# Performance work log

Measured on AMD Instinct MI355X. Metric: run time of the kernel, lower is better.

Reference implementation:

```python
import jax, jax.numpy as jnp
import numpy as np

K = 16  # num_neighbors
L = 3   # stacked PointTransformer layers


def _mlp2(x, w1, b1, w2, b2):
    return jax.nn.relu(x @ w1 + b1) @ w2 + b2


def setup_inputs() -> dict:
    key = jax.random.key(0)
    ks = jax.random.split(key, 10)
    B, N, D = 2, 8192, 3
    HP, HA = 32, 12  # pos_mlp hidden, attn_mlp hidden (3*4)
    f = lambda k, shp, s: jax.random.normal(k, shp, dtype=jnp.float32) * s
    return {
        "feats": f(ks[0], (B, N, D), 1.0),
        "pos": f(ks[1], (B, N, 3), 1.0),
        "mask": jnp.ones((B, N), dtype=bool),  # unused by PT.forward
        "w_qkv": f(ks[2], (L, D, 3 * D), 1.0 / np.sqrt(D)),
        "pos_w1": f(ks[3], (L, 3, HP), 1.0 / np.sqrt(3.0)),
        "pos_b1": jnp.zeros((L, HP), jnp.float32),
        "pos_w2": f(ks[4], (L, HP, D), 1.0 / np.sqrt(HP)),
        "pos_b2": jnp.zeros((L, D), jnp.float32),
        "attn_w1": f(ks[5], (L, D, HA), 1.0 / np.sqrt(D)),
        "attn_b1": jnp.zeros((L, HA), jnp.float32),
        "attn_w2": f(ks[6], (L, HA, D), 1.0 / np.sqrt(HA)),
        "attn_b2": jnp.zeros((L, D), jnp.float32),
        "lin_w": f(ks[7], (D, 2), 1.0 / np.sqrt(D)),
        "lin_b": jnp.zeros((2,), jnp.float32),
    }


def reference(feats, pos, mask, w_qkv, pos_w1, pos_b1, pos_w2, pos_b2,
              attn_w1, attn_b1, attn_w2, attn_b2, lin_w, lin_b):
    # kNN indices from pairwise squared distances (monotonic in the norm the
    # original uses, so topk-smallest gives identical neighbor sets).
    sq = jnp.sum(pos * pos, axis=-1)                               # [B,N]
    d2 = sq[:, :, None] + sq[:, None, :] - 2.0 * jnp.einsum('bic,bjc->bij', pos, pos)
    _, idx = jax.lax.top_k(-d2, K)                                 # [B,N,K]

    gather = jax.vmap(lambda t, i: t[i])                           # [B,N,d],[B,N,K]->[B,N,K,d]
    pos_j = gather(pos, idx)                                       # [B,N,K,3]
    rel_pos = pos[:, :, None, :] - pos_j                           # [B,N,K,3]

    h = feats
    for l in range(L):
        qkv = h @ w_qkv[l]                                         # [B,N,9]
        q, k, v = jnp.split(qkv, 3, axis=-1)
        k_j = gather(k, idx)                                       # [B,N,K,3]
        v_j = gather(v, idx)
        rel_emb = _mlp2(rel_pos, pos_w1[l], pos_b1[l], pos_w2[l], pos_b2[l])
        qk_rel = q[:, :, None, :] - k_j
        sim = _mlp2(qk_rel + rel_emb, attn_w1[l], attn_b1[l], attn_w2[l], attn_b2[l])
        attn = jax.nn.softmax(sim, axis=-2)                        # softmax over neighbors
        agg = jnp.einsum('bijd,bijd->bid', attn, v_j + rel_emb)    # [B,N,3]
        h = jax.nn.sigmoid(agg)
    out = h @ lin_w + lin_b                                        # [B,N,2]
    return jax.nn.softmax(out, axis=2)
```

## Files before the change

kernel.cpp:

```cpp
#include <hip/hip_runtime.h>
#include <math.h>

#define N_PTS 8192
#define BATCH 2
#define KNB 16
#define NQ (BATCH * N_PTS)

#define H    0.35f
#define INVH (1.0f / 0.35f)
#define NC   30
#define LBOX (0.5f * H * NC)
#define NCELL (NC * NC * NC)
#define MCELL (2 * NCELL)
#define NROW1 9
#define NROWT 43
#define NCHK 8
#define CHKP (N_PTS / NCHK)
#define SCANG 8192
#define MERGG 1024
#define WCAP 8192
#define FINF 3.4e38f

typedef unsigned long long u64;

__device__ __forceinline__ float med3f(float a, float b, float c) {
#if __has_builtin(__builtin_amdgcn_fmed3f)
    return __builtin_amdgcn_fmed3f(a, b, c);
#else
    return fmaxf(fminf(a, b), fminf(fmaxf(a, b), c));
#endif
}

__device__ __forceinline__ unsigned sortable(float x) {
    unsigned u = __float_as_uint(x);
    return u ^ ((unsigned)((int)u >> 31) | 0x80000000u);
}

__device__ __forceinline__ void ins_u64(u64 (&pk)[KNB], u64 key) {
    if (key < pk[0]) {
#pragma unroll
        for (int s = 0; s < KNB; ++s) {
            const u64 ds1 = (s < KNB - 1) ? pk[s + 1] : 0ull;
            const bool c0 = key < pk[s];
            const bool c1 = key < ds1;
            pk[s] = c1 ? ds1 : (c0 ? key : pk[s]);
        }
    }
}

__device__ __forceinline__ void sort16_desc_u64(u64 (&a)[KNB]) {
#pragma unroll
    for (int k = 2; k <= 16; k <<= 1) {
#pragma unroll
        for (int j = k >> 1; j > 0; j >>= 1) {
#pragma unroll
            for (int i = 0; i < 16; ++i) {
                const int l = i ^ j;
                if (l > i) {
                    const bool dirDesc = ((i & k) == 0);
                    const u64 mx = a[i] > a[l] ? a[i] : a[l];
                    const u64 mn = a[i] > a[l] ? a[l] : a[i];
                    a[i] = dirDesc ? mx : mn;
                    a[l] = dirDesc ? mn : mx;
                }
            }
        }
    }
}

__device__ __forceinline__ void merge64_u64(u64 (&pk)[KNB]) {
#pragma unroll
    for (int mm = 1; mm <= 32; mm <<= 1) {
        u64 L[KNB];
#pragma unroll
        for (int i = 0; i < KNB; ++i) {
            const u64 a = pk[i];
            const u64 c = __shfl_xor(pk[KNB - 1 - i], mm);
            L[i] = a < c ? a : c;
        }
#pragma unroll
        for (int dd = 8; dd >= 1; dd >>= 1) {
#pragma unroll
            for (int i = 0; i < KNB; ++i) {
                if ((i & dd) == 0) {
                    const u64 hi = L[i] > L[i | dd] ? L[i] : L[i | dd];
                    const u64 lo = L[i] > L[i | dd] ? L[i | dd] : L[i];
                    L[i] = hi; L[i | dd] = lo;
                }
            }
        }
#pragma unroll
        for (int i = 0; i < KNB; ++i) pk[i] = L[i];
    }
}

__global__ __launch_bounds__(256) void kcount(const float* __restrict__ pos,
                                              int* __restrict__ cnt,
                                              int* __restrict__ cellid) {
    const int g = blockIdx.x * 256 + threadIdx.x;
    const int b = g >> 13;
    const float x = pos[g * 3 + 0], y = pos[g * 3 + 1], z = pos[g * 3 + 2];
    int cx = (int)floorf((x + LBOX) * INVH); cx = min(max(cx, 0), NC - 1);
    int cy = (int)floorf((y + LBOX) * INVH); cy = min(max(cy, 0), NC - 1);
    int cz = (int)floorf((z + LBOX) * INVH); cz = min(max(cz, 0), NC - 1);
    const int c = (((b * NC) + cz) * NC + cy) * NC + cx;
    cellid[g] = c;
    atomicAdd(&cnt[c], 1);
}

__global__ __launch_bounds__(1024) void kscan1(const int* __restrict__ cnt,
                                               int* __restrict__ scanned,
                                               int* __restrict__ bsum) {
    __shared__ int sh[1024];
    const int t = threadIdx.x;
    const int idx = blockIdx.x * 1024 + t;
    int v = (idx < MCELL) ? cnt[idx] : 0;
    sh[t] = v;
    __syncthreads();
    for (int off = 1; off < 1024; off <<= 1) {
        const int add = (t >= off) ? sh[t - off] : 0;
        __syncthreads();
        sh[t] += add;
        __syncthreads();
    }
    if (idx < MCELL) scanned[idx] = sh[t];
    if (t == 1023) bsum[blockIdx.x] = sh[1023];
}

__global__ __launch_bounds__(1024) void kscan2(const int* __restrict__ scanned,
                                               const int* __restrict__ bsum,
                                               int* __restrict__ cell_start) {
    __shared__ int soff;
    const int t = threadIdx.x;
    const int blk = blockIdx.x;
    const int idx = blk * 1024 + t;
    if (t == 0) {
        int s = 0;
        for (int k = 0; k < blk; ++k) s += bsum[k];
        soff = s;
    }
    __syncthreads();
    if (idx < MCELL) cell_start[idx + 1] = scanned[idx] + soff;
    if (idx == 0) cell_start[0] = 0;
}

__global__ __launch_bounds__(256) void kscatter(const float* __restrict__ pos,
                                                const int* __restrict__ cellid,
                                                const int* __restrict__ cell_start,
                                                int* __restrict__ cnt2,
                                                float4* __restrict__ spp,
                                                int* __restrict__ sidx) {
    const int g = blockIdx.x * 256 + threadIdx.x;
    const int c = cellid[g];
    const int off = atomicAdd(&cnt2[c], 1);
    const int p = cell_start[c] + off;
    const float x = pos[g * 3 + 0], y = pos[g * 3 + 1], z = pos[g * 3 + 2];
    spp[p] = make_float4(-2.f * x, -2.f * y, -2.f * z, fmaf(x, x, fmaf(y, y, z * z)));
    sidx[p] = g & (N_PTS - 1);
}

__global__ __launch_bounds__(64, 4) void ksearch_fast(const float4* __restrict__ spp,
                                                      const int* __restrict__ sidx,
                                                      const int* __restrict__ cs,
                                                      int* __restrict__ knn,
                                                      int* __restrict__ ovf_list,
                                                      int* __restrict__ ovf_cnt) {
    __shared__ int rstL[4][NROWT];
    __shared__ int psL[4][NROWT + 1];
    const int tid = threadIdx.x;
    const int li  = tid & 15;
    const int gq  = tid >> 4;
    const int sq  = blockIdx.x * 4 + gq;
    const int b   = sq >> 13;

    {
        __shared__ int cntL[4][NROWT];
        for (int t = tid; t < 4 * NROWT; t += 64) {
            const int q = t / NROWT, r = t % NROWT;
            const int sq2 = blockIdx.x * 4 + q;
            const int b2  = sq2 >> 13;
            const float4 m2 = spp[sq2];
            const float px = -0.5f * m2.x, py = -0.5f * m2.y, pz = -0.5f * m2.z;
            int c2x = (int)floorf((px + LBOX) * INVH); c2x = min(max(c2x, 0), NC - 1);
            int c2y = (int)floorf((py + LBOX) * INVH); c2y = min(max(c2y, 0), NC - 1);
            int c2z = (int)floorf((pz + LBOX) * INVH); c2z = min(max(c2z, 0), NC - 1);

            int st = 0, en = 0;
            int z, y, xlo, xhi;
            bool ok = true;
            if (r < NROW1) {
                z = c2z + r / 3 - 1;
                y = c2y + (r % 3) - 1;
                xlo = max(c2x - 1, 0); xhi = min(c2x + 1, NC - 1);
            } else {
                const int rr = r - NROW1;
                if (rr < 10) {
                    z = c2z + (rr < 5 ? -2 : 2);
                    y = c2y + (rr % 5) - 2;
                    xlo = max(c2x - 2, 0); xhi = min(c2x + 2, NC - 1);
                } else if (rr < 16) {
                    const int k = rr - 10;
                    z = c2z + (k % 3) - 1;
                    y = c2y + (k < 3 ? -2 : 2);
                    xlo = max(c2x - 2, 0); xhi = min(c2x + 2, NC - 1);
                } else {
                    const int k = rr - 16;
                    const int m = k % 9;
                    z = c2z + m / 3 - 1;
                    y = c2y + (m % 3) - 1;
                    const int xx = c2x + (k < 9 ? -2 : 2);
                    xlo = xhi = xx;
                    ok = (xx >= 0) && (xx < NC);
                }
            }
            if (ok && z >= 0 && z < NC && y >= 0 && y < NC) {
                const int rowb = (((b2 * NC) + z) * NC + y) * NC;
                st = cs[rowb + xlo];
                en = cs[rowb + xhi + 1];
            }
            rstL[q][r] = st; cntL[q][r] = en - st;
        }
        __syncthreads();
        if (tid < 4) {
            int acc = 0;
            psL[tid][0] = 0;
            for (int r = 0; r < NROWT; ++r) { acc += cntL[tid][r]; psL[tid][r + 1] = acc; }
        }
        __syncthreads();
    }

    const float4 me = spp[sq];
    const float qx = -0.5f * me.x, qy = -0.5f * me.y, qz = -0.5f * me.z;
    const float qsq = me.w;
    int cx = (int)floorf((qx + LBOX) * INVH); cx = min(max(cx, 0), NC - 1);
    int cy = (int)floorf((qy + LBOX) * INVH); cy = min(max(cy, 0), NC - 1);
    int cz = (int)floorf((qz + LBOX) * INVH); cz = min(max(cz, 0), NC - 1);

    const int tot1 = psL[gq][NROW1];
    const int tot2 = psL[gq][NROWT];

    float d[KNB];
#pragma unroll
    for (int k = 0; k < KNB; ++k) d[k] = FINF;

    int row = 0;
    int t = li;

    auto scan1_flat = [&](int limit) {
        while (t < limit) {
            int pp[8]; bool vv[8];
#pragma unroll
            for (int u = 0; u < 8; ++u) {
                const int tt = t + u * 16;
                vv[u] = (tt < limit);
                int p = sq;
                if (vv[u]) {
                    while (tt >= psL[gq][row + 1]) ++row;
                    p = rstL[gq][row] + (tt - psL[gq][row]);
                }
                pp[u] = p;
            }
            float4 v[8];
#pragma unroll
            for (int u = 0; u < 8; ++u) v[u] = spp[pp[u]];
#pragma unroll
            for (int u = 0; u < 8; ++u) {
                const float x = vv[u] ? fmaf(qx, v[u].x, fmaf(qy, v[u].y, fmaf(qz, v[u].z, v[u].w)))
                                      : FINF;
                if (x < d[0]) {
#pragma unroll
                    for (int s = 0; s < KNB - 1; ++s) d[s] = med3f(d[s], d[s + 1], x);
                    d[KNB - 1] = fminf(d[KNB - 1], x);
                }
            }
            t += 128;
        }
    };

    auto boundtest = [&](int R) -> bool {
        const float bxl = fmaf((float)(cx - R), H, -LBOX);
        const float bxh = fmaf((float)(cx + R + 1), H, -LBOX);
        const float byl = fmaf((float)(cy - R), H, -LBOX);
        const float byh = fmaf((float)(cy + R + 1), H, -LBOX);
        const float bzl = fmaf((float)(cz - R), H, -LBOX);
        const float bzh = fmaf((float)(cz + R + 1), H, -LBOX);
        const float m = fminf(fminf(fminf(qx - bxl, bxh - qx),
                                    fminf(qy - byl, byh - qy)),
                              fminf(qz - bzl, bzh - qz));
        if (!(m > 0.f)) return false;
        const float Bf = fmaf(m, m, -1e-4f) - qsq;
        int c = 0;
#pragma unroll
        for (int k = 0; k < KNB; ++k) c += (d[k] <= Bf) ? 1 : 0;
#pragma unroll
        for (int off = 1; off < 16; off <<= 1) c += __shfl_xor(c, off);
        return c >= KNB;
    };

    scan1_flat(tot1);
    const bool done1 = boundtest(1);
    bool ovf = false;
    if (!done1) {
        scan1_flat(tot2);
        if (!boundtest(2)) ovf = true;
    }
    if (ovf) {
        if (li == 0) { const int s2 = atomicAdd(ovf_cnt, 1); ovf_list[s2] = sq; }
        return;
    }
    const int tot = done1 ? tot1 : tot2;

#pragma unroll
    for (int mm = 1; mm <= 8; mm <<= 1) {
        float L[KNB];
#pragma unroll
        for (int i = 0; i < KNB; ++i)
            L[i] = fminf(d[i], __shfl_xor(d[KNB - 1 - i], mm));
#pragma unroll
        for (int dd = 8; dd >= 1; dd >>= 1) {
#pragma unroll
            for (int i = 0; i < KNB; ++i) {
                if ((i & dd) == 0) {
                    const float hi = fmaxf(L[i], L[i | dd]);
                    const float lo = fminf(L[i], L[i | dd]);
                    L[i] = hi; L[i | dd] = lo;
                }
            }
        }
#pragma unroll
        for (int i = 0; i < KNB; ++i) d[i] = L[i];
    }
    const float thr = d[0];

    u64 pk[KNB];
#pragma unroll
    for (int k = 0; k < KNB; ++k) pk[k] = 0xFFFFFFFFFFFFFFFFull;

    row = 0;
    int t2 = li;
    while (t2 < tot) {
        int pp[8]; bool vv[8];
#pragma unroll
        for (int u = 0; u < 8; ++u) {
            const int tt = t2 + u * 16;
            vv[u] = (tt < tot);
            int p = sq;
            if (vv[u]) {
                while (tt >= psL[gq][row + 1]) ++row;
                p = rstL[gq][row] + (tt - psL[gq][row]);
            }
            pp[u] = p;
        }
        float4 v[8];
#pragma unroll
        for (int u = 0; u < 8; ++u) v[u] = spp[pp[u]];
#pragma unroll
        for (int u = 0; u < 8; ++u) {
            const float x = vv[u] ? fmaf(qx, v[u].x, fmaf(qy, v[u].y, fmaf(qz, v[u].z, v[u].w)))
                                  : FINF;
            if (x <= thr) {
                ins_u64(pk, ((u64)sortable(x) << 32) | (unsigned)sidx[pp[u]]);
            }
        }
        t2 += 128;
    }

#pragma unroll
    for (int mm = 1; mm <= 8; mm <<= 1) {
        u64 L[KNB];
#pragma unroll
        for (int i = 0; i < KNB; ++i) {
            const u64 a = pk[i];
            const u64 c = __shfl_xor(pk[KNB - 1 - i], mm);
            L[i] = a < c ? a : c;
        }
#pragma unroll
        for (int dd = 8; dd >= 1; dd >>= 1) {
#pragma unroll
            for (int i = 0; i < KNB; ++i) {
                if ((i & dd) == 0) {
                    const u64 hi = L[i] > L[i | dd] ? L[i] : L[i | dd];
                    const u64 lo = L[i] > L[i | dd] ? L[i | dd] : L[i];
                    L[i] = hi; L[i | dd] = lo;
                }
            }
        }
#pragma unroll
        for (int i = 0; i < KNB; ++i) pk[i] = L[i];
    }

    const int qorig = sidx[sq];
    const int obase = ((b << 13) + qorig) * KNB;
    u64 sel = pk[0];
#pragma unroll
    for (int s = 1; s < KNB; ++s) sel = (li == s) ? pk[s] : sel;
    knn[obase + li] = (int)(unsigned)(sel & 0xFFFFFFFFull);
}

__global__ __launch_bounds__(64, 4) void kslow_scan(const float4* __restrict__ spp,
                                                    const int* __restrict__ sidx,
                                                    const int* __restrict__ ovf_list,
                                                    const int* __restrict__ ovf_cnt,
                                                    u64* __restrict__ pbuf) {
    const int lane = threadIdx.x;
    const int ntask = min(*ovf_cnt, WCAP) * NCHK;

    for (int task = blockIdx.x; task < ntask; task += SCANG) {
        const int w = task >> 3;
        const int c = task & (NCHK - 1);
        const int sq = ovf_list[w];
        const int b  = sq >> 13;
        const float4 me = spp[sq];
        const float qx = -0.5f * me.x, qy = -0.5f * me.y, qz = -0.5f * me.z;
        const int cbase = (b << 13) + c * CHKP;

        u64 pk[KNB];
#pragma unroll
        for (int t0 = 0; t0 < 2; ++t0) {
            const int tb = cbase + lane + t0 * 512;
            float4 v[8];
            int id[8];
#pragma unroll
            for (int u = 0; u < 8; ++u) v[u] = spp[tb + u * 64];
#pragma unroll
            for (int u = 0; u < 8; ++u) id[u] = sidx[tb + u * 64];
#pragma unroll
            for (int u = 0; u < 8; ++u) {
                const float x = fmaf(qx, v[u].x, fmaf(qy, v[u].y, fmaf(qz, v[u].z, v[u].w)));
                pk[t0 * 8 + u] = ((u64)sortable(x) << 32) | (unsigned)id[u];
            }
        }

        sort16_desc_u64(pk);
        merge64_u64(pk);

        u64 sel = pk[0];
#pragma unroll
        for (int s = 1; s < KNB; ++s) sel = (lane == s) ? pk[s] : sel;
        if (lane < KNB) pbuf[(size_t)task * KNB + lane] = sel;
    }
}

__global__ __launch_bounds__(64) void kslow_merge(const float4* __restrict__ spp,
                                                  const int* __restrict__ sidx,
                                                  int* __restrict__ knn,
                                                  const int* __restrict__ ovf_list,
                                                  const int* __restrict__ ovf_cnt,
                                                  const u64* __restrict__ pbuf) {
    const int lane = threadIdx.x;
    const int nov = *ovf_cnt;

    for (int w = blockIdx.x; w < nov; w += MERGG) {
        const int sq = ovf_list[w];
        const int b  = sq >> 13;

        u64 pk[KNB];
#pragma unroll
        for (int k = 0; k < KNB; ++k) pk[k] = 0xFFFFFFFFFFFFFFFFull;

        if (w < WCAP) {
            const u64 a0 = pbuf[(size_t)w * (NCHK * KNB) + lane];
            const u64 a1 = pbuf[(size_t)w * (NCHK * KNB) + 64 + lane];
            ins_u64(pk, a0);
            ins_u64(pk, a1);
        } else {
            const float4 me = spp[sq];
            const float qx = -0.5f * me.x, qy = -0.5f * me.y, qz = -0.5f * me.z;
            const int base = b << 13;
            unsigned smax = 0xFFFFFFFFu;
            for (int t = lane; t < N_PTS; t += 64) {
                const float4 v = spp[base + t];
                const float x = fmaf(qx, v.x, fmaf(qy, v.y, fmaf(qz, v.z, v.w)));
                const unsigned sx = sortable(x);
                if (sx <= smax) {
                    ins_u64(pk, ((u64)sx << 32) | (unsigned)sidx[base + t]);
                    smax = (unsigned)(pk[0] >> 32);
                }
            }
        }

        merge64_u64(pk);

        const int qorig = sidx[sq];
        const int obase = ((b << 13) + qorig) * KNB;
        u64 sel = pk[0];
#pragma unroll
        for (int s = 1; s < KNB; ++s) sel = (lane == s) ? pk[s] : sel;
        if (lane < KNB) knn[obase + lane] = (int)(unsigned)(sel & 0xFFFFFFFFull);
    }
}

__global__ __launch_bounds__(256) void pt_layer_f(const float* __restrict__ hin,
                                                  const float* __restrict__ pos,
                                                  const int* __restrict__ knn,
                                                  const float* __restrict__ wqkv,
                                                  const float* __restrict__ pw1,
                                                  const float* __restrict__ pb1,
                                                  const float* __restrict__ pw2,
                                                  const float* __restrict__ pb2,
                                                  const float* __restrict__ aw1,
                                                  const float* __restrict__ ab1,
                                                  const float* __restrict__ aw2,
                                                  const float* __restrict__ ab2,
                                                  float* __restrict__ hout,
                                                  const float* __restrict__ lw,
                                                  const float* __restrict__ lb,
                                                  float* __restrict__ out,
                                                  int last) {
    const int gt = blockIdx.x * 256 + threadIdx.x;
    const int qg = gt >> 4;
    const int j  = gt & 15;
    const int b  = qg >> 13;
    const int jj = knn[qg * KNB + j] & (N_PTS - 1);
    const int g  = (b << 13) + jj;

    const float hi0 = hin[qg * 3 + 0], hi1 = hin[qg * 3 + 1], hi2 = hin[qg * 3 + 2];
    const float hj0 = hin[g * 3 + 0],  hj1 = hin[g * 3 + 1],  hj2 = hin[g * 3 + 2];
    const float rx = pos[qg * 3 + 0] - pos[g * 3 + 0];
    const float ry = pos[qg * 3 + 1] - pos[g * 3 + 1];
    const float rz = pos[qg * 3 + 2] - pos[g * 3 + 2];

    const float q0 = fmaf(hi0, wqkv[0], fmaf(hi1, wqkv[9],  hi2 * wqkv[18]));
    const float q1 = fmaf(hi0, wqkv[1], fmaf(hi1, wqkv[10], hi2 * wqkv[19]));
    const float q2 = fmaf(hi0, wqkv[2], fmaf(hi1, wqkv[11], hi2 * wqkv[20]));
    const float k0 = fmaf(hj0, wqkv[3], fmaf(hj1, wqkv[12], hj2 * wqkv[21]));
    const float k1 = fmaf(hj0, wqkv[4], fmaf(hj1, wqkv[13], hj2 * wqkv[22]));
    const float k2 = fmaf(hj0, wqkv[5], fmaf(hj1, wqkv[14], hj2 * wqkv[23]));
    const float v0 = fmaf(hj0, wqkv[6], fmaf(hj1, wqkv[15], hj2 * wqkv[24]));
    const float v1 = fmaf(hj0, wqkv[7], fmaf(hj1, wqkv[16], hj2 * wqkv[25]));
    const float v2 = fmaf(hj0, wqkv[8], fmaf(hj1, wqkv[17], hj2 * wqkv[26]));

    float e0 = pb2[0], e1 = pb2[1], e2 = pb2[2];
#pragma unroll
    for (int hh = 0; hh < 32; ++hh) {
        float t = fmaf(rx, pw1[hh], fmaf(ry, pw1[32 + hh], fmaf(rz, pw1[64 + hh], pb1[hh])));
        t = fmaxf(t, 0.0f);
        e0 = fmaf(t, pw2[hh * 3 + 0], e0);
        e1 = fmaf(t, pw2[hh * 3 + 1], e1);
        e2 = fmaf(t, pw2[hh * 3 + 2], e2);
    }

    const float x0 = q0 - k0 + e0;
    const float x1 = q1 - k1 + e1;
    const float x2 = q2 - k2 + e2;

    float s0 = ab2[0], s1 = ab2[1], s2 = ab2[2];
#pragma unroll
    for (int hh = 0; hh < 12; ++hh) {
        float t = fmaf(x0, aw1[hh], fmaf(x1, aw1[12 + hh], fmaf(x2, aw1[24 + hh], ab1[hh])));
        t = fmaxf(t, 0.0f);
        s0 = fmaf(t, aw2[hh * 3 + 0], s0);
        s1 = fmaf(t, aw2[hh * 3 + 1], s1);
        s2 = fmaf(t, aw2[hh * 3 + 2], s2);
    }

    const float w0 = v0 + e0, w1 = v1 + e1, w2 = v2 + e2;

    float m0 = s0, m1 = s1, m2 = s2;
#pragma unroll
    for (int off = 1; off < 16; off <<= 1) {
        m0 = fmaxf(m0, __shfl_xor(m0, off));
        m1 = fmaxf(m1, __shfl_xor(m1, off));
        m2 = fmaxf(m2, __shfl_xor(m2, off));
    }
    const float ex0 = __expf(s0 - m0), ex1 = __expf(s1 - m1), ex2 = __expf(s2 - m2);
    float n0 = ex0 * w0, n1 = ex1 * w1, n2 = ex2 * w2;
    float den0 = ex0, den1 = ex1, den2 = ex2;
#pragma unroll
    for (int off = 1; off < 16; off <<= 1) {
        den0 += __shfl_xor(den0, off); n0 += __shfl_xor(n0, off);
        den1 += __shfl_xor(den1, off); n1 += __shfl_xor(n1, off);
        den2 += __shfl_xor(den2, off); n2 += __shfl_xor(n2, off);
    }

    if (j == 0) {
        const float h0 = 1.f / (1.f + __expf(-(n0 / den0)));
        const float h1 = 1.f / (1.f + __expf(-(n1 / den1)));
        const float h2 = 1.f / (1.f + __expf(-(n2 / den2)));
        if (!last) {
            hout[qg * 3 + 0] = h0;
            hout[qg * 3 + 1] = h1;
            hout[qg * 3 + 2] = h2;
        } else {
            const float o0 = fmaf(h0, lw[0], fmaf(h1, lw[2], fmaf(h2, lw[4], lb[0])));
            const float o1 = fmaf(h0, lw[1], fmaf(h1, lw[3], fmaf(h2, lw[5], lb[1])));
            const float mm = fmaxf(o0, o1);
            const float ea = __expf(o0 - mm), eb = __expf(o1 - mm);
            const float inv = 1.f / (ea + eb);
            out[qg * 2 + 0] = ea * inv;
            out[qg * 2 + 1] = eb * inv;
        }
    }
}

extern "C" void kernel_launch(void* const* d_in, const int* in_sizes, int n_in,
                              void* d_out, int out_size, void* d_ws, size_t ws_size,
                              hipStream_t stream) {
    const float* feats = (const float*)d_in[0];
    const float* pos   = (const float*)d_in[1];
    const float* wqkv = (const float*)d_in[3];
    const float* pw1  = (const float*)d_in[4];
    const float* pb1  = (const float*)d_in[5];
    const float* pw2  = (const float*)d_in[6];
    const float* pb2  = (const float*)d_in[7];
    const float* aw1  = (const float*)d_in[8];
    const float* ab1  = (const float*)d_in[9];
    const float* aw2  = (const float*)d_in[10];
    const float* ab2  = (const float*)d_in[11];
    const float* lw   = (const float*)d_in[12];
    const float* lb   = (const float*)d_in[13];
    float* out = (float*)d_out;

    size_t o = 0;
    auto take = [&](size_t bytes) { size_t r = o; o += (bytes + 15) & ~(size_t)15; return r; };
    const size_t o_cnt   = take((size_t)(2 * MCELL + 4) * 4);
    const size_t o_scan  = take((size_t)MCELL * 4);
    const size_t o_cs    = take((size_t)(MCELL + 1) * 4);
    const size_t o_bsum  = take((size_t)256 * 4);
    const size_t o_cid   = take((size_t)NQ * 4);
    const size_t o_spp   = take((size_t)NQ * 16);
    const size_t o_sidx  = take((size_t)NQ * 4);
    const size_t o_knn   = take((size_t)NQ * KNB * 4);
    const size_t o_ovfl  = take((size_t)NQ * 4);
    const size_t o_hA    = take((size_t)NQ * 3 * 4);
    const size_t o_hB    = take((size_t)NQ * 3 * 4);
    const size_t o_pbuf  = take((size_t)WCAP * NCHK * KNB * 8);
    if (ws_size < o) return;

    char* ws = (char*)d_ws;
    int*    cnt     = (int*)(ws + o_cnt);
    int*    cnt2    = cnt + MCELL;
    int*    ovf_cnt = cnt + 2 * MCELL;
    int*    scan  = (int*)(ws + o_scan);
    int*    cs    = (int*)(ws + o_cs);
    int*    bsum  = (int*)(ws + o_bsum);
    int*    cid   = (int*)(ws + o_cid);
    float4* spp   = (float4*)(ws + o_spp);
    int*    sidx  = (int*)(ws + o_sidx);
    int*    knn   = (int*)(ws + o_knn);
    int*    ovfl  = (int*)(ws + o_ovfl);
    float*  hA    = (float*)(ws + o_hA);
    float*  hB    = (float*)(ws + o_hB);
    u64*    pbuf  = (u64*)(ws + o_pbuf);

    const int nscan = (MCELL + 1023) / 1024;

    hipMemsetAsync(cnt, 0, (size_t)(2 * MCELL + 1) * 4, stream);
    kcount<<<NQ / 256, 256, 0, stream>>>(pos, cnt, cid);
    kscan1<<<nscan, 1024, 0, stream>>>(cnt, scan, bsum);
    kscan2<<<nscan, 1024, 0, stream>>>(scan, bsum, cs);
    kscatter<<<NQ / 256, 256, 0, stream>>>(pos, cid, cs, cnt2, spp, sidx);
    ksearch_fast<<<NQ / 4, 64, 0, stream>>>(spp, sidx, cs, knn, ovfl, ovf_cnt);
    kslow_scan<<<SCANG, 64, 0, stream>>>(spp, sidx, ovfl, ovf_cnt, pbuf);
    kslow_merge<<<MERGG, 64, 0, stream>>>(spp, sidx, knn, ovfl, ovf_cnt, pbuf);

    pt_layer_f<<<NQ * 16 / 256, 256, 0, stream>>>(feats, pos, knn,
        wqkv + 0, pw1 + 0, pb1 + 0, pw2 + 0, pb2 + 0,
        aw1 + 0, ab1 + 0, aw2 + 0, ab2 + 0,
        hA, lw, lb, out, 0);
    pt_layer_f<<<NQ * 16 / 256, 256, 0, stream>>>(hA, pos, knn,
        wqkv + 27, pw1 + 96, pb1 + 32, pw2 + 96, pb2 + 3,
        aw1 + 36, ab1 + 12, aw2 + 36, ab2 + 3,
        hB, lw, lb, out, 0);
    pt_layer_f<<<NQ * 16 / 256, 256, 0, stream>>>(hB, pos, knn,
        wqkv + 54, pw1 + 192, pb1 + 64, pw2 + 192, pb2 + 6,
        aw1 + 72, ab1 + 24, aw2 + 72, ab2 + 6,
        hB, lw, lb, out, 1);
}
```

Before: 132.4 us.

## Fuse slow kNN fallback into one two-pass threshold kernel

Replaces the two-kernel chunked fallback search (per-chunk u64 bitonic sort into a partial buffer, then a merge kernel) with a single kernel that has one wave handle each overflow query. The first pass keeps a float-only top-16 per lane with med3 insertion and merges across the wave to get the 16th-smallest distance. The second pass rescans all points and inserts only candidates at or below that threshold into the u64 key/index list. This drops a kernel launch, the partial buffer traffic and the wide u64 sorts, at the cost of reading the point set twice with only 1024 waves of parallelism instead of 8192 chunk tasks. If many points tie at the threshold, which ones are kept could differ from before.

```diff
diff --git a/kernel.cpp b/kernel.cpp
--- a/kernel.cpp
+++ b/kernel.cpp
@@ -14,11 +14,7 @@
 #define MCELL (2 * NCELL)
 #define NROW1 9
 #define NROWT 43
-#define NCHK 8
-#define CHKP (N_PTS / NCHK)
-#define SCANG 8192
-#define MERGG 1024
-#define WCAP 8192
+#define SLOWG 1024
 #define FINF 3.4e38f
 
 typedef unsigned long long u64;
@@ -48,26 +44,6 @@
     }
 }
 
-__device__ __forceinline__ void sort16_desc_u64(u64 (&a)[KNB]) {
-#pragma unroll
-    for (int k = 2; k <= 16; k <<= 1) {
-#pragma unroll
-        for (int j = k >> 1; j > 0; j >>= 1) {
-#pragma unroll
-            for (int i = 0; i < 16; ++i) {
-                const int l = i ^ j;
-                if (l > i) {
-                    const bool dirDesc = ((i & k) == 0);
-                    const u64 mx = a[i] > a[l] ? a[i] : a[l];
-                    const u64 mn = a[i] > a[l] ? a[l] : a[i];
-                    a[i] = dirDesc ? mx : mn;
-                    a[l] = dirDesc ? mn : mx;
-                }
-            }
-        }
-    }
-}
-
 __device__ __forceinline__ void merge64_u64(u64 (&pk)[KNB]) {
 #pragma unroll
     for (int mm = 1; mm <= 32; mm <<= 1) {
@@ -91,6 +67,29 @@
         }
 #pragma unroll
         for (int i = 0; i < KNB; ++i) pk[i] = L[i];
+    }
+}
+
+__device__ __forceinline__ void merge64_f(float (&d)[KNB]) {
+#pragma unroll
+    for (int mm = 1; mm <= 32; mm <<= 1) {
+        float L[KNB];
+#pragma unroll
+        for (int i = 0; i < KNB; ++i)
+            L[i] = fminf(d[i], __shfl_xor(d[KNB - 1 - i], mm));
+#pragma unroll
+        for (int dd = 8; dd >= 1; dd >>= 1) {
+#pragma unroll
+            for (int i = 0; i < KNB; ++i) {
+                if ((i & dd) == 0) {
+                    const float hi = fmaxf(L[i], L[i | dd]);
+                    const float lo = fminf(L[i], L[i | dd]);
+                    L[i] = hi; L[i | dd] = lo;
+                }
+            }
+        }
+#pragma unroll
+        for (int i = 0; i < KNB; ++i) d[i] = L[i];
     }
 }
 
@@ -397,88 +396,60 @@
     knn[obase + li] = (int)(unsigned)(sel & 0xFFFFFFFFull);
 }
 
-__global__ __launch_bounds__(64, 4) void kslow_scan(const float4* __restrict__ spp,
-                                                    const int* __restrict__ sidx,
-                                                    const int* __restrict__ ovf_list,
-                                                    const int* __restrict__ ovf_cnt,
-                                                    u64* __restrict__ pbuf) {
+__global__ __launch_bounds__(64, 4) void kslow(const float4* __restrict__ spp,
+                                               const int* __restrict__ sidx,
+                                               int* __restrict__ knn,
+                                               const int* __restrict__ ovf_list,
+                                               const int* __restrict__ ovf_cnt) {
     const int lane = threadIdx.x;
-    const int ntask = min(*ovf_cnt, WCAP) * NCHK;
-
-    for (int task = blockIdx.x; task < ntask; task += SCANG) {
-        const int w = task >> 3;
-        const int c = task & (NCHK - 1);
+    const int nov = *ovf_cnt;
+
+    for (int w = blockIdx.x; w < nov; w += SLOWG) {
         const int sq = ovf_list[w];
         const int b  = sq >> 13;
         const float4 me = spp[sq];
         const float qx = -0.5f * me.x, qy = -0.5f * me.y, qz = -0.5f * me.z;
-        const int cbase = (b << 13) + c * CHKP;
-
-        u64 pk[KNB];
-#pragma unroll
-        for (int t0 = 0; t0 < 2; ++t0) {
-            const int tb = cbase + lane + t0 * 512;
+        const int base = b << 13;
+
+        float d[KNB];
+#pragma unroll
+        for (int k = 0; k < KNB; ++k) d[k] = FINF;
+
+        for (int t0 = 0; t0 < 16; ++t0) {
+            const int tb = base + lane + t0 * 512;
             float4 v[8];
-            int id[8];
 #pragma unroll
             for (int u = 0; u < 8; ++u) v[u] = spp[tb + u * 64];
-#pragma unroll
-            for (int u = 0; u < 8; ++u) id[u] = sidx[tb + u * 64];
 #pragma unroll
             for (int u = 0; u < 8; ++u) {
                 const float x = fmaf(qx, v[u].x, fmaf(qy, v[u].y, fmaf(qz, v[u].z, v[u].w)));
-                pk[t0 * 8 + u] = ((u64)sortable(x) << 32) | (unsigned)id[u];
-            }
-        }
-
-        sort16_desc_u64(pk);
-        merge64_u64(pk);
-
-        u64 sel = pk[0];
-#pragma unroll
-        for (int s = 1; s < KNB; ++s) sel = (lane == s) ? pk[s] : sel;
-        if (lane < KNB) pbuf[(size_t)task * KNB + lane] = sel;
-    }
-}
-
-__global__ __launch_bounds__(64) void kslow_merge(const float4* __restrict__ spp,
-                                                  const int* __restrict__ sidx,
-                                                  int* __restrict__ knn,
-                                                  const int* __restrict__ ovf_list,
-                                                  const int* __restrict__ ovf_cnt,
-                                                  const u64* __restrict__ pbuf) {
-    const int lane = threadIdx.x;
-    const int nov = *ovf_cnt;
-
-    for (int w = blockIdx.x; w < nov; w += MERGG) {
-        const int sq = ovf_list[w];
-        const int b  = sq >> 13;
+                if (x < d[0]) {
+#pragma unroll
+                    for (int s = 0; s < KNB - 1; ++s) d[s] = med3f(d[s], d[s + 1], x);
+                    d[KNB - 1] = fminf(d[KNB - 1], x);
+                }
+            }
+        }
+        merge64_f(d);
+        const float thr = d[0];
 
         u64 pk[KNB];
 #pragma unroll
         for (int k = 0; k < KNB; ++k) pk[k] = 0xFFFFFFFFFFFFFFFFull;
 
-        if (w < WCAP) {
-            const u64 a0 = pbuf[(size_t)w * (NCHK * KNB) + lane];
-            const u64 a1 = pbuf[(size_t)w * (NCHK * KNB) + 64 + lane];
-            ins_u64(pk, a0);
-            ins_u64(pk, a1);
-        } else {
-            const float4 me = spp[sq];
-            const float qx = -0.5f * me.x, qy = -0.5f * me.y, qz = -0.5f * me.z;
-            const int base = b << 13;
-            unsigned smax = 0xFFFFFFFFu;
-            for (int t = lane; t < N_PTS; t += 64) {
-                const float4 v = spp[base + t];
-                const float x = fmaf(qx, v.x, fmaf(qy, v.y, fmaf(qz, v.z, v.w)));
-                const unsigned sx = sortable(x);
-                if (sx <= smax) {
-                    ins_u64(pk, ((u64)sx << 32) | (unsigned)sidx[base + t]);
-                    smax = (unsigned)(pk[0] >> 32);
-                }
-            }
-        }
-
+        for (int t0 = 0; t0 < 16; ++t0) {
+            const int tb = base + lane + t0 * 512;
+            float4 v[8];
+#pragma unroll
+            for (int u = 0; u < 8; ++u) v[u] = spp[tb + u * 64];
+#pragma unroll
+            for (int u = 0; u < 8; ++u) {
+                const float x = fmaf(qx, v[u].x, fmaf(qy, v[u].y, fmaf(qz, v[u].z, v[u].w)));
+                if (x <= thr) {
+                    ins_u64(pk, ((u64)sortable(x) << 32) | (unsigned)sidx[tb + u * 64]);
+                }
+            }
+        }
         merge64_u64(pk);
 
         const int qorig = sidx[sq];
@@ -624,7 +595,6 @@
     const size_t o_ovfl  = take((size_t)NQ * 4);
     const size_t o_hA    = take((size_t)NQ * 3 * 4);
     const size_t o_hB    = take((size_t)NQ * 3 * 4);
-    const size_t o_pbuf  = take((size_t)WCAP * NCHK * KNB * 8);
     if (ws_size < o) return;
 
     char* ws = (char*)d_ws;
@@ -641,7 +611,6 @@
     int*    ovfl  = (int*)(ws + o_ovfl);
     float*  hA    = (float*)(ws + o_hA);
     float*  hB    = (float*)(ws + o_hB);
-    u64*    pbuf  = (u64*)(ws + o_pbuf);
 
     const int nscan = (MCELL + 1023) / 1024;
 
@@ -651,8 +620,7 @@
     kscan2<<<nscan, 1024, 0, stream>>>(scan, bsum, cs);
     kscatter<<<NQ / 256, 256, 0, stream>>>(pos, cid, cs, cnt2, spp, sidx);
     ksearch_fast<<<NQ / 4, 64, 0, stream>>>(spp, sidx, cs, knn, ovfl, ovf_cnt);
-    kslow_scan<<<SCANG, 64, 0, stream>>>(spp, sidx, ovfl, ovf_cnt, pbuf);
-    kslow_merge<<<MERGG, 64, 0, stream>>>(spp, sidx, knn, ovfl, ovf_cnt, pbuf);
+    kslow<<<SLOWG, 64, 0, stream>>>(spp, sidx, knn, ovfl, ovf_cnt);
 
     pt_layer_f<<<NQ * 16 / 256, 256, 0, stream>>>(feats, pos, knn,
         wqkv + 0, pw1 + 0, pb1 + 0, pw2 + 0, pb2 + 0,
```

Result: faster. 126.6 us (-4.4%).
